# Performance work log

Measured on AMD Instinct MI355X. Metric: run time of the kernel, lower is better.

The kernel has to match this reference:

```python
import jax, jax.numpy as jnp
import numpy as np

B, S = 256, 256          # batch, seq_len
V, E = 8000, 128         # char vocab, char emb dim
HC, HW = 128, 256        # char_lstm_hid_dim, word_lstm_hid_dim


def setup_inputs() -> dict:
    key = jax.random.key(0)
    ks = jax.random.split(key, 20)
    n = lambda k, sh: (jax.random.normal(k, sh) * 0.05).astype(jnp.float32)
    return {
        "insts": jax.random.randint(ks[0], (B, S), 0, V),
        "golds": jax.random.randint(ks[1], (B, S), 0, 3),
        "emb": n(ks[2], (V, E)),
        "Wih_f": n(ks[3], (4 * HC, E)), "Whh_f": n(ks[4], (4 * HC, HC)), "b_f": n(ks[5], (4 * HC,)),
        "Wih_b": n(ks[6], (4 * HC, E)), "Whh_b": n(ks[7], (4 * HC, HC)), "b_b": n(ks[8], (4 * HC,)),
        "sub_Wih": n(ks[9], (4 * HW, 2 * HC)), "sub_Whh": n(ks[10], (4 * HW, HW)), "sub_b": n(ks[11], (4 * HW,)),
        "wrd_Wih": n(ks[12], (4 * HW, HW)), "wrd_Whh": n(ks[13], (4 * HW, HW)), "wrd_b": n(ks[14], (4 * HW,)),
        "cls_W": n(ks[15], (2, HW + 2 * HC)), "cls_b": n(ks[16], (2,)),
    }


def _cell(x, h, c, Wih, Whh, b):
    # PyTorch LSTMCell convention: gates ordered i, f, g, o
    g = x @ Wih.T + h @ Whh.T + b
    i, f, gg, o = jnp.split(g, 4, axis=-1)
    c = jax.nn.sigmoid(f) * c + jax.nn.sigmoid(i) * jnp.tanh(gg)
    h = jax.nn.sigmoid(o) * jnp.tanh(c)
    return h, c


def reference(insts, golds, emb, Wih_f, Whh_f, b_f, Wih_b, Whh_b, b_b,
              sub_Wih, sub_Whh, sub_b, wrd_Wih, wrd_Whh, wrd_b, cls_W, cls_b):
    # --- CharEncoder: embedding + BiLSTM, seq-first output [S, B, 2*HC] ---
    x = emb[insts].transpose(1, 0, 2)  # [S, B, E]
    z = jnp.zeros((B, HC), x.dtype)

    def mk_step(Wih, Whh, b):
        def step(hc, xt):
            h, c = _cell(xt, hc[0], hc[1], Wih, Whh, b)
            return (h, c), h
        return step

    _, hf = jax.lax.scan(mk_step(Wih_f, Whh_f, b_f), (z, z), x)
    _, hb = jax.lax.scan(mk_step(Wih_b, Whh_b, b_b), (z, z), x[::-1])
    chars = jnp.concatenate([hf, hb[::-1]], axis=-1)  # [S, B, 2*HC]

    # subword LSTM input at step t is chars[t-1] (zeros at t=0)
    sub_in = jnp.concatenate([jnp.zeros((1, B, 2 * HC), chars.dtype), chars[:-1]], axis=0)

    smap = jnp.array([1, 2, 2], jnp.int32)  # subword_action_map
    wmap = jnp.array([0, 1, 1], jnp.int32)  # word_action_map
    bidx = jnp.arange(B)

    # stacks: read state at pos, write new state at pos+1, then pos += op
    sh = jnp.zeros((2 * S + 2, B, HW), chars.dtype)
    sc = jnp.zeros((2 * S + 2, B, HW), chars.dtype)
    wh = jnp.zeros((S + 1, B, HW), chars.dtype)
    wc = jnp.zeros((S + 1, B, HW), chars.dtype)
    sp = jnp.zeros((B,), jnp.int32)
    wp = jnp.zeros((B,), jnp.int32)

    def step(carry, inp):
        sh, sc, sp, wh, wc, wp = carry
        xs, xc, g = inp  # subword input [B,2HC], classifier char feat [B,2HC], gold op [B]
        h1, c1 = _cell(xs, sh[sp, bidx], sc[sp, bidx], sub_Wih, sub_Whh, sub_b)
        sh = sh.at[sp + 1, bidx].set(h1)
        sc = sc.at[sp + 1, bidx].set(c1)
        h2, c2 = _cell(h1, wh[wp, bidx], wc[wp, bidx], wrd_Wih, wrd_Whh, wrd_b)
        wh = wh.at[wp + 1, bidx].set(h2)
        wc = wc.at[wp + 1, bidx].set(c2)
        out = jnp.concatenate([h2, xc], axis=-1) @ cls_W.T + cls_b  # [B, 2]
        return (sh, sc, sp + smap[g], wh, wc, wp + wmap[g]), out

    _, outs = jax.lax.scan(step, (sh, sc, sp, wh, wc, wp),
                           (sub_in, chars, golds.T.astype(jnp.int32)))
    return outs.transpose(1, 0, 2)  # [B, S, 2]
```

## Files before the change

kernel.cpp:

```cpp
#include <hip/hip_runtime.h>

#define S_LEN 256
#define BATCH 256

typedef _Float16 f16;
typedef _Float16 f16x8 __attribute__((ext_vector_type(8)));
typedef _Float16 f16x4 __attribute__((ext_vector_type(4)));
typedef float f32x4 __attribute__((ext_vector_type(4)));

__device__ inline float sigf(float x) { return 1.f / (1.f + __expf(-x)); }
__device__ inline float tanhf2(float x) { return 2.f * sigf(2.f * x) - 1.f; }

__global__ void k_convert(const float* __restrict__ w3, const float* __restrict__ w4,
                          const float* __restrict__ w6, const float* __restrict__ w7,
                          const float* __restrict__ w9, const float* __restrict__ w10,
                          const float* __restrict__ w12, const float* __restrict__ w13,
                          f16* __restrict__ dst) {
  int i = blockIdx.x * blockDim.x + threadIdx.x;
  const int n = 1310720;
  for (; i < n; i += gridDim.x * blockDim.x) {
    float v;
    if (i < 262144) {
      int m = i >> 16, j = i & 65535;
      v = (m == 0 ? w3 : m == 1 ? w4 : m == 2 ? w6 : w7)[j];
    } else {
      int k = i - 262144;
      int m = k >> 18, j = k & 262143;
      v = (m == 0 ? w9 : m == 1 ? w10 : m == 2 ? w12 : w13)[j];
    }
    dst[i] = (f16)v;
  }
}

__global__ void k_zero(unsigned* __restrict__ p, int n) {
  int i = blockIdx.x * blockDim.x + threadIdx.x;
  for (; i < n; i += gridDim.x * blockDim.x) p[i] = 0u;
}

__global__ void k_gather(const int* __restrict__ insts, const float* __restrict__ emb,
                         f16* __restrict__ Xf) {
  int gid = blockIdx.x * blockDim.x + threadIdx.x;
  int row = gid >> 5;
  int ch = gid & 31;
  int t = row >> 8, b = row & 255;
  int v = insts[b * S_LEN + t];
  const float* src = emb + (size_t)v * 128 + ch * 4;
  f16x4 d;
  d[0] = (f16)src[0]; d[1] = (f16)src[1]; d[2] = (f16)src[2]; d[3] = (f16)src[3];
  *(f16x4*)&Xf[(size_t)row * 128 + ch * 4] = d;
}

__global__ __launch_bounds__(512, 2)
void k_char(const f16* __restrict__ wbuf, const f16* __restrict__ Xf,
            const float* __restrict__ bias_f, const float* __restrict__ bias_b,
            f16* __restrict__ chars) {
  const int bwd = blockIdx.x >> 4;
  const int m0 = (blockIdx.x & 15) * 16;
  const f16* Wih = wbuf + (bwd ? 131072 : 0);
  const f16* Whh = wbuf + (bwd ? 196608 : 65536);
  const float* bias = bwd ? bias_b : bias_f;

  const int tid = threadIdx.x;
  const int lane = tid & 63;
  const int wave = tid >> 6;
  const int gw = wave >> 1;
  const int u0 = (wave & 1) * 64;
  const int l15 = lane & 15;
  const int kb = (lane >> 4) * 8;

  __shared__ f16 xs[2][16][136];
  __shared__ f16 hs[16][136];
  __shared__ float gex[16][520];

  f32x4 fih[4][4], fhh[4][4];
  float bv[4];
#pragma unroll
  for (int tt = 0; tt < 4; ++tt) {
    int col = gw * 128 + u0 + tt * 16 + l15;
    bv[tt] = bias[col];
#pragma unroll
    for (int ks = 0; ks < 4; ++ks) {
      fih[tt][ks] = *(const volatile f32x4*)&Wih[col * 128 + ks * 32 + kb];
      fhh[tt][ks] = *(const volatile f32x4*)&Whh[col * 128 + ks * 32 + kb];
    }
  }

  for (int i = tid; i < 16 * 136; i += 512) ((f16*)hs)[i] = (f16)0.f;
  {
    int mm = tid >> 5, cc = (tid & 31) * 4;
    int t_in = bwd ? (S_LEN - 1) : 0;
    *(f16x4*)&xs[0][mm][cc] =
        *(const f16x4*)&Xf[(size_t)t_in * BATCH * 128 + (m0 + mm) * 128 + cc];
  }
  float cst[4] = {0.f, 0.f, 0.f, 0.f};
  const int cm = tid >> 5;
  const int cu = (tid & 31) * 4;
  __syncthreads();

  for (int s = 0; s < S_LEN; ++s) {
    const int par = s & 1;
    f32x4 acc[4];
#pragma unroll
    for (int tt = 0; tt < 4; ++tt) { f32x4 a = {bv[tt], bv[tt], bv[tt], bv[tt]}; acc[tt] = a; }
#pragma unroll
    for (int ks = 0; ks < 4; ++ks) {
      f16x8 ax = *(const f16x8*)&xs[par][l15][ks * 32 + kb];
      f16x8 ah = *(const f16x8*)&hs[l15][ks * 32 + kb];
#pragma unroll
      for (int tt = 0; tt < 4; ++tt) {
        acc[tt] = __builtin_amdgcn_mfma_f32_16x16x32_f16(
            ax, __builtin_bit_cast(f16x8, fih[tt][ks]), acc[tt], 0, 0, 0);
        acc[tt] = __builtin_amdgcn_mfma_f32_16x16x32_f16(
            ah, __builtin_bit_cast(f16x8, fhh[tt][ks]), acc[tt], 0, 0, 0);
      }
    }
    f16x4 xreg;
    const int sn = s + 1;
    if (sn < S_LEN) {
      int t_in = bwd ? (S_LEN - 1 - sn) : sn;
      xreg = *(const f16x4*)&Xf[(size_t)t_in * BATCH * 128 + (m0 + cm) * 128 + cu];
    }
#pragma unroll
    for (int tt = 0; tt < 4; ++tt) {
      int col = gw * 128 + u0 + tt * 16 + l15;
#pragma unroll
      for (int r = 0; r < 4; ++r) gex[(lane >> 4) * 4 + r][col] = acc[tt][r];
    }
    __syncthreads();
    f16x4 hv;
#pragma unroll
    for (int qq = 0; qq < 4; ++qq) {
      int u = cu + qq;
      float gi = gex[cm][u], gf = gex[cm][128 + u], gg = gex[cm][256 + u], go = gex[cm][384 + u];
      float c = sigf(gf) * cst[qq] + sigf(gi) * tanhf2(gg);
      cst[qq] = c;
      hv[qq] = (f16)(sigf(go) * tanhf2(c));
    }
    {
      int t_in = bwd ? (S_LEN - 1 - s) : s;
      int cbase = bwd ? (128 + cu) : cu;
      *(f16x4*)&chars[(size_t)t_in * BATCH * 256 + (m0 + cm) * 256 + cbase] = hv;
      *(f16x4*)&hs[cm][cu] = hv;
      if (sn < S_LEN) *(f16x4*)&xs[par ^ 1][cm][cu] = xreg;
    }
    __syncthreads();
  }
}

__global__ __launch_bounds__(256, 1)
void k_subword(const f16* __restrict__ wbuf, const f16* __restrict__ chars,
               const int* __restrict__ golds,
               const float* __restrict__ b_sub, const float* __restrict__ b_wrd,
               f16* __restrict__ h1buf, f16* __restrict__ whbuf,
               unsigned* __restrict__ flags, f16* __restrict__ H2) {
  const int team = blockIdx.x >> 4;
  const int q = blockIdx.x & 15;
  const int m0 = team * 16;
  const int h0 = q * 16;
  const int tid = threadIdx.x, lane = tid & 63, wave = tid >> 6;
  const int l15 = lane & 15, kb = (lane >> 4) * 8;

  const f16* sWih = wbuf + 262144;
  const f16* sWhh = wbuf + 524288;
  const f16* wWih = wbuf + 786432;
  const f16* wWhh = wbuf + 1048576;

  __shared__ f16 xs_s[16][264];
  __shared__ f16 h1_s[16][264];
  __shared__ f16 wh_s[16][264];
  __shared__ float gexS[16][68];
  __shared__ float gexW[16][68];
  __shared__ int golds_s[16][256];

  f32x4 fsi[8], fsh[8], fwi[8], fwh[8];
  const int wr = wave * 256 + h0 + l15;
#pragma unroll
  for (int ks = 0; ks < 8; ++ks) {
    fsi[ks] = *(const volatile f32x4*)&sWih[wr * 256 + ks * 32 + kb];
    fsh[ks] = *(const volatile f32x4*)&sWhh[wr * 256 + ks * 32 + kb];
    fwi[ks] = *(const volatile f32x4*)&wWih[wr * 256 + ks * 32 + kb];
    fwh[ks] = *(const volatile f32x4*)&wWhh[wr * 256 + ks * 32 + kb];
  }
  const float bS = b_sub[wr], bW = b_wrd[wr];

  for (int i = tid; i < 16 * 256; i += 256)
    golds_s[i >> 8][i & 255] = golds[(m0 + (i >> 8)) * S_LEN + (i & 255)];
  for (int i = tid; i < 16 * 264; i += 256) {
    ((f16*)xs_s)[i] = (f16)0.f;
    ((f16*)h1_s)[i] = (f16)0.f;
    ((f16*)wh_s)[i] = (f16)0.f;
  }
  const int cm = tid >> 4, cj = tid & 15;
  const int sr = tid >> 4;
  const int sc = (tid & 15) * 16;
  float c_sub = 0.f, c_wrd = 0.f;
  __syncthreads();

  for (int i = 0; i <= S_LEN; ++i) {
    const bool doW = (i > 0), doS = (i < S_LEN);

    f16x4 chpre[4];
    if (doS) {
#pragma unroll
      for (int p = 0; p < 4; ++p)
        chpre[p] = *(const f16x4*)&chars[(size_t)i * BATCH * 256 + (m0 + sr) * 256 + sc + p * 4];
    }

    f32x4 accW = {bW, bW, bW, bW};
    f32x4 accS = {bS, bS, bS, bS};
    if (doW) {
#pragma unroll
      for (int ks = 0; ks < 8; ++ks) {
        f16x8 a1 = *(const f16x8*)&h1_s[l15][ks * 32 + kb];
        f16x8 aw = *(const f16x8*)&wh_s[l15][ks * 32 + kb];
        accW = __builtin_amdgcn_mfma_f32_16x16x32_f16(
            a1, __builtin_bit_cast(f16x8, fwi[ks]), accW, 0, 0, 0);
        accW = __builtin_amdgcn_mfma_f32_16x16x32_f16(
            aw, __builtin_bit_cast(f16x8, fwh[ks]), accW, 0, 0, 0);
      }
    }
    if (doS) {
      const bool keep = (i > 0) && (golds_s[l15][i > 0 ? i - 1 : 0] == 0);
      f16x8 z8 = {};
#pragma unroll
      for (int ks = 0; ks < 8; ++ks) {
        f16x8 axv = *(const f16x8*)&xs_s[l15][ks * 32 + kb];
        f16x8 a1 = *(const f16x8*)&h1_s[l15][ks * 32 + kb];
        a1 = keep ? a1 : z8;
        accS = __builtin_amdgcn_mfma_f32_16x16x32_f16(
            axv, __builtin_bit_cast(f16x8, fsi[ks]), accS, 0, 0, 0);
        accS = __builtin_amdgcn_mfma_f32_16x16x32_f16(
            a1, __builtin_bit_cast(f16x8, fsh[ks]), accS, 0, 0, 0);
      }
    }
#pragma unroll
    for (int r = 0; r < 4; ++r) {
      if (doW) gexW[(lane >> 4) * 4 + r][wave * 16 + l15] = accW[r];
      if (doS) gexS[(lane >> 4) * 4 + r][wave * 16 + l15] = accS[r];
    }
    __syncthreads();

    const int gprev = (i > 0) ? golds_s[cm][i - 1] : 1;
    if (doW) {
      float gi = gexW[cm][cj], gf = gexW[cm][16 + cj], gg = gexW[cm][32 + cj],
            go = gexW[cm][48 + cj];
      float c2 = sigf(gf) * c_wrd + sigf(gi) * tanhf2(gg);
      float h2 = sigf(go) * tanhf2(c2);
      bool adv = (gprev != 0);
      if (adv) c_wrd = c2;
      float whold = (float)wh_s[cm][h0 + cj];
      f16 whnew = (f16)(adv ? h2 : whold);
      H2[(size_t)(i - 1) * BATCH * 256 + (m0 + cm) * 256 + h0 + cj] = (f16)h2;
      if (doS)
        __hip_atomic_store(
            (unsigned short*)&whbuf[(size_t)(i & 1) * 65536 + (m0 + cm) * 256 + h0 + cj],
            __builtin_bit_cast(unsigned short, whnew), __ATOMIC_RELAXED,
            __HIP_MEMORY_SCOPE_AGENT);
    }
    if (doS) {
      float gi = gexS[cm][cj], gf = gexS[cm][16 + cj], gg = gexS[cm][32 + cj],
            go = gexS[cm][48 + cj];
      float cp = (gprev == 0) ? c_sub : 0.f;
      float c1 = sigf(gf) * cp + sigf(gi) * tanhf2(gg);
      c_sub = c1;
      f16 h1 = (f16)(sigf(go) * tanhf2(c1));
      __hip_atomic_store(
          (unsigned short*)&h1buf[(size_t)(i & 1) * 65536 + (m0 + cm) * 256 + h0 + cj],
          __builtin_bit_cast(unsigned short, h1), __ATOMIC_RELAXED, __HIP_MEMORY_SCOPE_AGENT);
    }
    __syncthreads();

    if (doS) {
      if (tid == 0)
        __hip_atomic_store(&flags[(team * 16 + q) * 16], (unsigned)(i + 1), __ATOMIC_RELAXED,
                           __HIP_MEMORY_SCOPE_AGENT);
      if (tid < 64) {
        const unsigned tgt = (unsigned)(i + 1);
        while (true) {
          unsigned v = tgt;
          if (lane < 16)
            v = __hip_atomic_load(&flags[(team * 16 + lane) * 16], __ATOMIC_RELAXED,
                                  __HIP_MEMORY_SCOPE_AGENT);
          if (__all(v >= tgt)) break;
          __builtin_amdgcn_s_sleep(1);
        }
      }
      asm volatile("" ::: "memory");
      __syncthreads();
#pragma unroll
      for (int p = 0; p < 4; ++p) {
        int c4 = sc + p * 4;
        unsigned long long v1 = __hip_atomic_load(
            (const unsigned long long*)&h1buf[(size_t)(i & 1) * 65536 + (m0 + sr) * 256 + c4],
            __ATOMIC_RELAXED, __HIP_MEMORY_SCOPE_AGENT);
        unsigned long long v2 = __hip_atomic_load(
            (const unsigned long long*)&whbuf[(size_t)(i & 1) * 65536 + (m0 + sr) * 256 + c4],
            __ATOMIC_RELAXED, __HIP_MEMORY_SCOPE_AGENT);
        *(f16x4*)&h1_s[sr][c4] = __builtin_bit_cast(f16x4, v1);
        *(f16x4*)&wh_s[sr][c4] = __builtin_bit_cast(f16x4, v2);
        *(f16x4*)&xs_s[sr][c4] = chpre[p];
      }
      __syncthreads();
    }
  }
}

__global__ __launch_bounds__(256)
void k_cls(const f16* __restrict__ H2, const f16* __restrict__ chars,
           const float* __restrict__ clsW, const float* __restrict__ clsb,
           float* __restrict__ out) {
  const int w = (blockIdx.x << 2) | (threadIdx.x >> 6);
  const int lane = threadIdx.x & 63;
  const int t = w >> 8, b = w & 255;
  const f16* h2p = H2 + (size_t)w * 256;
  const f16* chp = chars + (size_t)w * 256;
  float s0 = 0.f, s1 = 0.f;
  f16x4 hv = *(const f16x4*)&h2p[lane * 4];
  f16x4 cv = *(const f16x4*)&chp[lane * 4];
#pragma unroll
  for (int qq = 0; qq < 4; ++qq) {
    int u = lane * 4 + qq;
    s0 += (float)hv[qq] * clsW[u] + (float)cv[qq] * clsW[256 + u];
    s1 += (float)hv[qq] * clsW[512 + u] + (float)cv[qq] * clsW[768 + u];
  }
#pragma unroll
  for (int off = 32; off >= 1; off >>= 1) {
    s0 += __shfl_down(s0, off);
    s1 += __shfl_down(s1, off);
  }
  if (lane == 0) {
    out[((size_t)b * S_LEN + t) * 2 + 0] = s0 + clsb[0];
    out[((size_t)b * S_LEN + t) * 2 + 1] = s1 + clsb[1];
  }
}

extern "C" void kernel_launch(void* const* d_in, const int* in_sizes, int n_in,
                              void* d_out, int out_size, void* d_ws, size_t ws_size,
                              hipStream_t stream) {
  const int* insts = (const int*)d_in[0];
  const int* golds = (const int*)d_in[1];
  const float* emb = (const float*)d_in[2];
  const float* wihf = (const float*)d_in[3];
  const float* whhf = (const float*)d_in[4];
  const float* bf = (const float*)d_in[5];
  const float* wihb = (const float*)d_in[6];
  const float* whhb = (const float*)d_in[7];
  const float* bb = (const float*)d_in[8];
  const float* swih = (const float*)d_in[9];
  const float* swhh = (const float*)d_in[10];
  const float* sb = (const float*)d_in[11];
  const float* wwih = (const float*)d_in[12];
  const float* wwhh = (const float*)d_in[13];
  const float* wb = (const float*)d_in[14];
  const float* clsW = (const float*)d_in[15];
  const float* clsb = (const float*)d_in[16];
  float* out = (float*)d_out;

  const size_t OFF_W = 0;
  const size_t OFF_XF = 2621440;
  const size_t OFF_CHARS = 19398656;
  const size_t OFF_H2 = 52953088;
  const size_t OFF_H1 = 86507520;
  const size_t OFF_WH = 86769664;
  const size_t OFF_FLAGS = 87031808;
  const size_t TOTAL = 87048192;
  if (ws_size < TOTAL) return;

  char* ws = (char*)d_ws;
  f16* wbuf = (f16*)(ws + OFF_W);
  f16* Xf = (f16*)(ws + OFF_XF);
  f16* chars = (f16*)(ws + OFF_CHARS);
  f16* H2 = (f16*)(ws + OFF_H2);
  f16* h1buf = (f16*)(ws + OFF_H1);
  f16* whbuf = (f16*)(ws + OFF_WH);
  unsigned* flags = (unsigned*)(ws + OFF_FLAGS);

  hipLaunchKernelGGL(k_convert, dim3(1024), dim3(256), 0, stream, wihf, whhf, wihb, whhb,
                     swih, swhh, wwih, wwhh, wbuf);
  hipLaunchKernelGGL(k_zero, dim3(256), dim3(256), 0, stream, (unsigned*)(ws + OFF_H1),
                     135168);
  hipLaunchKernelGGL(k_gather, dim3(8192), dim3(256), 0, stream, insts, emb, Xf);
  hipLaunchKernelGGL(k_char, dim3(32), dim3(512), 0, stream, wbuf, Xf, bf, bb, chars);
  hipLaunchKernelGGL(k_subword, dim3(256), dim3(256), 0, stream, wbuf, chars, golds, sb, wb,
                     h1buf, whbuf, flags, H2);
  hipLaunchKernelGGL(k_cls, dim3(16384), dim3(256), 0, stream, H2, chars, clsW, clsb, out);
}
```

Baseline: 1.359 ms.

## Replace flag barrier with step-tagged data publication and team-major chars layout

The cross-block exchange in the subword kernel now packs a step counter together with the h1 and word-h values into one 64-bit word per element. Consumers poll their own 16 words until every tag matches the current step. This removes the separate flag array, the spin-wait barrier and one __syncthreads per step, so each block waits only for the data it reads. The chars buffer is also reordered team-major so each team's per-step reads are contiguous, at the cost of more polling traffic on shared global memory.

```diff
diff --git a/kernel.cpp b/kernel.cpp
--- a/kernel.cpp
+++ b/kernel.cpp
@@ -55,7 +55,8 @@
             const float* __restrict__ bias_f, const float* __restrict__ bias_b,
             f16* __restrict__ chars) {
   const int bwd = blockIdx.x >> 4;
-  const int m0 = (blockIdx.x & 15) * 16;
+  const int teamc = blockIdx.x & 15;
+  const int m0 = teamc * 16;
   const f16* Wih = wbuf + (bwd ? 131072 : 0);
   const f16* Whh = wbuf + (bwd ? 196608 : 65536);
   const float* bias = bwd ? bias_b : bias_f;
@@ -139,7 +140,7 @@
     {
       int t_in = bwd ? (S_LEN - 1 - s) : s;
       int cbase = bwd ? (128 + cu) : cu;
-      *(f16x4*)&chars[(size_t)t_in * BATCH * 256 + (m0 + cm) * 256 + cbase] = hv;
+      *(f16x4*)&chars[(size_t)(((teamc * S_LEN + t_in) * 16 + cm) * 256) + cbase] = hv;
       *(f16x4*)&hs[cm][cu] = hv;
       if (sn < S_LEN) *(f16x4*)&xs[par ^ 1][cm][cu] = xreg;
     }
@@ -151,8 +152,7 @@
 void k_subword(const f16* __restrict__ wbuf, const f16* __restrict__ chars,
                const int* __restrict__ golds,
                const float* __restrict__ b_sub, const float* __restrict__ b_wrd,
-               f16* __restrict__ h1buf, f16* __restrict__ whbuf,
-               unsigned* __restrict__ flags, f16* __restrict__ H2) {
+               unsigned long long* __restrict__ pub, f16* __restrict__ H2) {
   const int team = blockIdx.x >> 4;
   const int q = blockIdx.x & 15;
   const int m0 = team * 16;
@@ -193,17 +193,19 @@
   const int cm = tid >> 4, cj = tid & 15;
   const int sr = tid >> 4;
   const int sc = (tid & 15) * 16;
-  float c_sub = 0.f, c_wrd = 0.f;
+  float c_sub = 0.f, c_wrd = 0.f, wh_reg = 0.f;
   __syncthreads();
 
   for (int i = 0; i <= S_LEN; ++i) {
     const bool doW = (i > 0), doS = (i < S_LEN);
+    const int slotbase = ((i & 1) * 16 + team) << 12;
 
     f16x4 chpre[4];
     if (doS) {
 #pragma unroll
       for (int p = 0; p < 4; ++p)
-        chpre[p] = *(const f16x4*)&chars[(size_t)i * BATCH * 256 + (m0 + sr) * 256 + sc + p * 4];
+        chpre[p] = *(const f16x4*)&chars[(size_t)(((team * S_LEN + i) * 16 + sr) * 256) +
+                                         sc + p * 4];
     }
 
     f32x4 accW = {bW, bW, bW, bW};
@@ -247,15 +249,8 @@
       float c2 = sigf(gf) * c_wrd + sigf(gi) * tanhf2(gg);
       float h2 = sigf(go) * tanhf2(c2);
       bool adv = (gprev != 0);
-      if (adv) c_wrd = c2;
-      float whold = (float)wh_s[cm][h0 + cj];
-      f16 whnew = (f16)(adv ? h2 : whold);
+      if (adv) { c_wrd = c2; wh_reg = h2; }
       H2[(size_t)(i - 1) * BATCH * 256 + (m0 + cm) * 256 + h0 + cj] = (f16)h2;
-      if (doS)
-        __hip_atomic_store(
-            (unsigned short*)&whbuf[(size_t)(i & 1) * 65536 + (m0 + cm) * 256 + h0 + cj],
-            __builtin_bit_cast(unsigned short, whnew), __ATOMIC_RELAXED,
-            __HIP_MEMORY_SCOPE_AGENT);
     }
     if (doS) {
       float gi = gexS[cm][cj], gf = gexS[cm][16 + cj], gg = gexS[cm][32 + cj],
@@ -264,42 +259,48 @@
       float c1 = sigf(gf) * cp + sigf(gi) * tanhf2(gg);
       c_sub = c1;
       f16 h1 = (f16)(sigf(go) * tanhf2(c1));
-      __hip_atomic_store(
-          (unsigned short*)&h1buf[(size_t)(i & 1) * 65536 + (m0 + cm) * 256 + h0 + cj],
-          __builtin_bit_cast(unsigned short, h1), __ATOMIC_RELAXED, __HIP_MEMORY_SCOPE_AGENT);
-    }
-    __syncthreads();
+      unsigned long long val =
+          ((unsigned long long)(i + 1) << 48) |
+          ((unsigned long long)__builtin_bit_cast(unsigned short, h1) << 16) |
+          (unsigned long long)__builtin_bit_cast(unsigned short, (f16)wh_reg);
+      __hip_atomic_store(&pub[slotbase + cm * 256 + h0 + cj], val, __ATOMIC_RELAXED,
+                         __HIP_MEMORY_SCOPE_AGENT);
+      asm volatile("" ::: "memory");
+    }
 
     if (doS) {
-      if (tid == 0)
-        __hip_atomic_store(&flags[(team * 16 + q) * 16], (unsigned)(i + 1), __ATOMIC_RELAXED,
-                           __HIP_MEMORY_SCOPE_AGENT);
-      if (tid < 64) {
-        const unsigned tgt = (unsigned)(i + 1);
-        while (true) {
-          unsigned v = tgt;
-          if (lane < 16)
-            v = __hip_atomic_load(&flags[(team * 16 + lane) * 16], __ATOMIC_RELAXED,
-                                  __HIP_MEMORY_SCOPE_AGENT);
-          if (__all(v >= tgt)) break;
-          __builtin_amdgcn_s_sleep(1);
+      const unsigned long long tgt = (unsigned long long)(i + 1);
+      const int base = slotbase + sr * 256 + sc;
+      unsigned long long w[16];
+#pragma unroll
+      for (int k = 0; k < 16; ++k) w[k] = 0ull;
+      while (true) {
+        bool ok = true;
+#pragma unroll
+        for (int k = 0; k < 16; ++k) {
+          if ((w[k] >> 48) != tgt) {
+            w[k] = __hip_atomic_load(&pub[base + k], __ATOMIC_RELAXED,
+                                     __HIP_MEMORY_SCOPE_AGENT);
+            ok &= ((w[k] >> 48) == tgt);
+          }
         }
-      }
-      asm volatile("" ::: "memory");
-      __syncthreads();
-#pragma unroll
-      for (int p = 0; p < 4; ++p) {
-        int c4 = sc + p * 4;
-        unsigned long long v1 = __hip_atomic_load(
-            (const unsigned long long*)&h1buf[(size_t)(i & 1) * 65536 + (m0 + sr) * 256 + c4],
-            __ATOMIC_RELAXED, __HIP_MEMORY_SCOPE_AGENT);
-        unsigned long long v2 = __hip_atomic_load(
-            (const unsigned long long*)&whbuf[(size_t)(i & 1) * 65536 + (m0 + sr) * 256 + c4],
-            __ATOMIC_RELAXED, __HIP_MEMORY_SCOPE_AGENT);
-        *(f16x4*)&h1_s[sr][c4] = __builtin_bit_cast(f16x4, v1);
-        *(f16x4*)&wh_s[sr][c4] = __builtin_bit_cast(f16x4, v2);
-        *(f16x4*)&xs_s[sr][c4] = chpre[p];
-      }
+        if (ok) break;
+        __builtin_amdgcn_s_sleep(1);
+      }
+#pragma unroll
+      for (int half = 0; half < 2; ++half) {
+        union { unsigned short s[8]; f16x8 v; } uh, uw;
+#pragma unroll
+        for (int k = 0; k < 8; ++k) {
+          unsigned long long v = w[half * 8 + k];
+          uh.s[k] = (unsigned short)((v >> 16) & 0xffffu);
+          uw.s[k] = (unsigned short)(v & 0xffffu);
+        }
+        *(f16x8*)&h1_s[sr][sc + half * 8] = uh.v;
+        *(f16x8*)&wh_s[sr][sc + half * 8] = uw.v;
+      }
+#pragma unroll
+      for (int p = 0; p < 4; ++p) *(f16x4*)&xs_s[sr][sc + p * 4] = chpre[p];
       __syncthreads();
     }
   }
@@ -313,7 +314,7 @@
   const int lane = threadIdx.x & 63;
   const int t = w >> 8, b = w & 255;
   const f16* h2p = H2 + (size_t)w * 256;
-  const f16* chp = chars + (size_t)w * 256;
+  const f16* chp = chars + (size_t)(((b >> 4) * S_LEN + t) * 16 + (b & 15)) * 256;
   float s0 = 0.f, s1 = 0.f;
   f16x4 hv = *(const f16x4*)&h2p[lane * 4];
   f16x4 cv = *(const f16x4*)&chp[lane * 4];
@@ -358,11 +359,9 @@
 
   const size_t OFF_W = 0;
   const size_t OFF_XF = 2621440;
+  const size_t OFF_PUB = OFF_XF + 4194304;
   const size_t OFF_CHARS = 19398656;
   const size_t OFF_H2 = 52953088;
-  const size_t OFF_H1 = 86507520;
-  const size_t OFF_WH = 86769664;
-  const size_t OFF_FLAGS = 87031808;
   const size_t TOTAL = 87048192;
   if (ws_size < TOTAL) return;
 
@@ -371,17 +370,15 @@
   f16* Xf = (f16*)(ws + OFF_XF);
   f16* chars = (f16*)(ws + OFF_CHARS);
   f16* H2 = (f16*)(ws + OFF_H2);
-  f16* h1buf = (f16*)(ws + OFF_H1);
-  f16* whbuf = (f16*)(ws + OFF_WH);
-  unsigned* flags = (unsigned*)(ws + OFF_FLAGS);
+  unsigned long long* pub = (unsigned long long*)(ws + OFF_PUB);
 
   hipLaunchKernelGGL(k_convert, dim3(1024), dim3(256), 0, stream, wihf, whhf, wihb, whhb,
                      swih, swhh, wwih, wwhh, wbuf);
-  hipLaunchKernelGGL(k_zero, dim3(256), dim3(256), 0, stream, (unsigned*)(ws + OFF_H1),
-                     135168);
   hipLaunchKernelGGL(k_gather, dim3(8192), dim3(256), 0, stream, insts, emb, Xf);
   hipLaunchKernelGGL(k_char, dim3(32), dim3(512), 0, stream, wbuf, Xf, bf, bb, chars);
+  hipLaunchKernelGGL(k_zero, dim3(512), dim3(256), 0, stream, (unsigned*)(ws + OFF_PUB),
+                     262144);
   hipLaunchKernelGGL(k_subword, dim3(256), dim3(256), 0, stream, wbuf, chars, golds, sb, wb,
-                     h1buf, whbuf, flags, H2);
+                     pub, H2);
   hipLaunchKernelGGL(k_cls, dim3(16384), dim3(256), 0, stream, H2, chars, clsW, clsb, out);
 }
```

Result: slower. 2.285 ms (+68.1%).
